# Performance work log

Measured on AMD Instinct MI355X. Metric: run time of the kernel, lower is better.

## Reference

```python
import jax, jax.numpy as jnp
import numpy as np

B, S, D, H, DFF = 4, 1024, 1024, 16, 4096
MAX_LEN = 1024
DK = D // H
EPS = 1e-5


def _ln(x, g, b):
    m = jnp.mean(x, axis=-1, keepdims=True)
    v = jnp.mean(jnp.square(x - m), axis=-1, keepdims=True)
    return (x - m) / jnp.sqrt(v + EPS) * g + b


def setup_inputs() -> dict:
    key = jax.random.key(0)
    ks = jax.random.split(key, 16)
    s = 0.02
    inp = {
        "x": jax.random.normal(ks[0], (B, S, D), jnp.float32),
        "wq": jax.random.normal(ks[1], (D, D), jnp.float32) * s,
        "bq": jnp.zeros((D,), jnp.float32),
        "wk": jax.random.normal(ks[2], (D, D), jnp.float32) * s,
        "bk": jnp.zeros((D,), jnp.float32),
        "wv": jax.random.normal(ks[3], (D, D), jnp.float32) * s,
        "bv": jnp.zeros((D,), jnp.float32),
        "wo": jax.random.normal(ks[4], (D, D), jnp.float32) * s,
        "bo": jnp.zeros((D,), jnp.float32),
        "rel_table": jax.random.normal(ks[5], (2 * MAX_LEN - 1, H), jnp.float32) * s,
        "ln1_g": jnp.ones((D,), jnp.float32),
        "ln1_b": jnp.zeros((D,), jnp.float32),
        "w1": jax.random.normal(ks[6], (D, DFF), jnp.float32) * s,
        "b1": jnp.zeros((DFF,), jnp.float32),
        "w2": jax.random.normal(ks[7], (DFF, D), jnp.float32) * s,
        "b2": jnp.zeros((D,), jnp.float32),
        "ln2_g": jnp.ones((D,), jnp.float32),
        "ln2_b": jnp.zeros((D,), jnp.float32),
        "mask": jnp.ones((B, 1, 1, S), jnp.int32),
    }
    return inp


def reference(x, wq, bq, wk, bk, wv, bv, wo, bo, rel_table,
              ln1_g, ln1_b, w1, b1, w2, b2, ln2_g, ln2_b, mask):
    # --- multi-head attention with relative position bias (post-LN encoder layer, eval mode) ---
    q = (x @ wq + bq).reshape(B, S, H, DK).transpose(0, 2, 1, 3)  # [B,H,S,dk]
    k = (x @ wk + bk).reshape(B, S, H, DK).transpose(0, 2, 1, 3)
    v = (x @ wv + bv).reshape(B, S, H, DK).transpose(0, 2, 1, 3)

    scores = jnp.einsum('bhqd,bhkd->bhqk', q, k) / jnp.sqrt(jnp.float32(DK))

    # relative position bias: table[(q - k + max_len - 1).clip] -> [1,H,S,S]
    coords = jnp.arange(S)[:, None] - jnp.arange(S)[None, :] + (MAX_LEN - 1)
    coords = jnp.clip(coords, 0, 2 * MAX_LEN - 2)
    bias = rel_table[coords]              # [S,S,H]
    scores = scores + bias.transpose(2, 0, 1)[None]

    scores = jnp.where(mask == 0, jnp.float32(-1e9), scores)
    attn = jax.nn.softmax(scores, axis=-1)
    ctx = jnp.einsum('bhqk,bhkd->bhqd', attn, v)
    ctx = ctx.transpose(0, 2, 1, 3).reshape(B, S, D)
    attn_out = ctx @ wo + bo

    x1 = _ln(x + attn_out, ln1_g, ln1_b)

    ff = jax.nn.relu(x1 @ w1 + b1) @ w2 + b2
    return _ln(x1 + ff, ln2_g, ln2_b)
```

## Files before the change

kernel.cpp:

```cpp
#include <hip/hip_runtime.h>
#include <hip/hip_bf16.h>

typedef __hip_bfloat16 bf16;
typedef __attribute__((ext_vector_type(8))) short short8;
typedef __attribute__((ext_vector_type(4))) float f32x4;

#define LOG2E 1.4426950408889634f

typedef const __attribute__((address_space(1))) void* gptr_t;
typedef __attribute__((address_space(3))) void* sptr_t;

__device__ __forceinline__ void async16(void* lds, const void* g) {
  __builtin_amdgcn_global_load_lds((gptr_t)g, (sptr_t)lds, 16, 0, 0);
}

__device__ __forceinline__ float bf2f(unsigned short u) {
  union { unsigned int i; float f; } c; c.i = ((unsigned int)u) << 16; return c.f;
}


__global__ __launch_bounds__(256) void prep_all(
    const float* __restrict__ x, const float* __restrict__ bq,
    const float* __restrict__ bk, const float* __restrict__ bv,
    const float* __restrict__ wq, const float* __restrict__ wk,
    const float* __restrict__ wv, const float* __restrict__ wo,
    const float* __restrict__ w1, const float* __restrict__ w2,
    bf16* __restrict__ xb, float* __restrict__ bqkv,
    bf16* __restrict__ dqkv, bf16* __restrict__ dwo,
    bf16* __restrict__ dw1, bf16* __restrict__ dw2) {
  const int bid = blockIdx.x;
  if (bid < 4096) {
    int i = (bid * 256 + threadIdx.x) * 4;
    float4 v = *(const float4*)(x + i);
    bf16 h4[4] = {__float2bfloat16(v.x), __float2bfloat16(v.y),
                  __float2bfloat16(v.z), __float2bfloat16(v.w)};
    *(uint2*)((unsigned short*)xb + i) = *(uint2*)h4;
    return;
  }
  if (bid == 16384) {
#pragma unroll
    for (int j = 0; j < 12; ++j) {
      int i = j * 256 + threadIdx.x;
      bqkv[i] = (i < 1024) ? bq[i] : (i < 2048 ? bk[i - 1024] : bv[i - 2048]);
    }
    return;
  }
  __shared__ float tl[32][33];
  const int tid = bid - 4096;
  const float* s;
  bf16* d;
  int NN, KK, n0, k0;
  if (tid < 4096) {
    int m = tid >> 10, tile = tid & 1023;
    s = m == 0 ? wq : m == 1 ? wk : m == 2 ? wv : wo;
    d = m < 3 ? dqkv + (size_t)m * 1024 * 1024 : dwo;
    NN = 1024; KK = 1024;
    n0 = (tile & 31) * 32; k0 = (tile >> 5) * 32;
  } else if (tid < 8192) {
    int tile = tid - 4096;
    s = w1; d = dw1; NN = 4096; KK = 1024;
    n0 = (tile & 127) * 32; k0 = (tile >> 7) * 32;
  } else {
    int tile = tid - 8192;
    s = w2; d = dw2; NN = 1024; KK = 4096;
    n0 = (tile & 31) * 32; k0 = (tile >> 5) * 32;
  }
  const int tx = threadIdx.x & 31, ty = threadIdx.x >> 5;
#pragma unroll
  for (int j = 0; j < 4; ++j)
    tl[ty + j * 8][tx] = s[(size_t)(k0 + ty + j * 8) * NN + n0 + tx];
  __syncthreads();
#pragma unroll
  for (int j = 0; j < 4; ++j)
    d[(size_t)(n0 + ty + j * 8) * KK + k0 + tx] =
        __float2bfloat16(tl[tx][ty + j * 8]);
}


template <int RELU, int VT>
__global__ __launch_bounds__(256) void gemm_bt(
    const bf16* __restrict__ A, const bf16* __restrict__ Bt,
    const float* __restrict__ bias, bf16* __restrict__ C,
    bf16* __restrict__ vt, int M, int N, int K) {
  __shared__ bf16 As[2][128 * 64];
  __shared__ bf16 Bs[2][128 * 64];
  const int t = threadIdx.x;
  const int w = t >> 6, l = t & 63;
  const int m0 = blockIdx.x * 128, n0 = blockIdx.y * 128;
  const int wr = (w >> 1) * 64, wc = (w & 1) * 64;
  const int srow = l >> 3, scol = l & 7;
  const int lm = l & 15, lq = l >> 4;

  f32x4 acc[4][4];
#pragma unroll
  for (int i = 0; i < 4; ++i)
#pragma unroll
    for (int j = 0; j < 4; ++j) acc[i][j] = (f32x4){0.f, 0.f, 0.f, 0.f};

  auto stage = [&](int k0, int d) {
#pragma unroll
    for (int p = 0; p < 4; ++p) {
      int row = p * 32 + w * 8 + srow;
      int gc = scol ^ (row & 7);
      async16(&As[d][(p * 32 + w * 8) * 64], A + (size_t)(m0 + row) * K + k0 + gc * 8);
      async16(&Bs[d][(p * 32 + w * 8) * 64], Bt + (size_t)(n0 + row) * K + k0 + gc * 8);
    }
  };

  stage(0, 0);
  const int niter = K >> 6;
  for (int it = 0; it < niter; ++it) {
    const int d = it & 1;
    __syncthreads();
    short8 af[2][4], bfr[2][4];
#pragma unroll
    for (int kk = 0; kk < 2; ++kk)
#pragma unroll
      for (int mi = 0; mi < 4; ++mi) {
        int rowa = wr + mi * 16 + lm;
        af[kk][mi] = *(const short8*)&As[d][rowa * 64 + (((kk * 4 + lq) ^ (rowa & 7)) << 3)];
        int rowb = wc + mi * 16 + lm;
        bfr[kk][mi] = *(const short8*)&Bs[d][rowb * 64 + (((kk * 4 + lq) ^ (rowb & 7)) << 3)];
      }
    if (it + 1 < niter) stage((it + 1) << 6, d ^ 1);
#pragma unroll
    for (int kk = 0; kk < 2; ++kk)
#pragma unroll
      for (int mi = 0; mi < 4; ++mi)
#pragma unroll
        for (int ni = 0; ni < 4; ++ni)
          acc[mi][ni] = __builtin_amdgcn_mfma_f32_16x16x32_bf16(
              af[kk][mi], bfr[kk][ni], acc[mi][ni], 0, 0, 0);
  }

#pragma unroll
  for (int mi = 0; mi < 4; ++mi)
#pragma unroll
    for (int ni = 0; ni < 4; ++ni) {
      int col = n0 + wc + ni * 16 + lm;
      int row0 = m0 + wr + mi * 16 + lq * 4;
      float bv = bias[col];
      float v[4];
#pragma unroll
      for (int r = 0; r < 4; ++r) {
        v[r] = acc[mi][ni][r] + bv;
        if (RELU) v[r] = fmaxf(v[r], 0.f);
        C[(size_t)(row0 + r) * N + col] = __float2bfloat16(v[r]);
      }
      if (VT && col >= 2048) {
        int vcol = col - 2048;
        int bh = (row0 >> 10) * 16 + (vcol >> 6);
        int dk = vcol & 63;
        int s = row0 & 1023;
        bf16 h4[4] = {__float2bfloat16(v[0]), __float2bfloat16(v[1]),
                      __float2bfloat16(v[2]), __float2bfloat16(v[3])};
        *(uint2*)&vt[((size_t)bh * 64 + dk) * 1024 + s] = *(uint2*)h4;
      }
    }
}

__global__ __launch_bounds__(256) void gemm_bt_splitk(
    const bf16* __restrict__ A, const bf16* __restrict__ Bt,
    bf16* __restrict__ P, int M, int N, int lda, int KS) {
  __shared__ bf16 As[2][128 * 64];
  __shared__ bf16 Bs[2][128 * 64];
  const int t = threadIdx.x;
  const int w = t >> 6, l = t & 63;
  const int m0 = blockIdx.x * 128, n0 = blockIdx.y * 128;
  const int kstart = blockIdx.z * KS;
  const int wr = (w >> 1) * 64, wc = (w & 1) * 64;
  const int srow = l >> 3, scol = l & 7;
  const int lm = l & 15, lq = l >> 4;

  f32x4 acc[4][4];
#pragma unroll
  for (int i = 0; i < 4; ++i)
#pragma unroll
    for (int j = 0; j < 4; ++j) acc[i][j] = (f32x4){0.f, 0.f, 0.f, 0.f};

  auto stage = [&](int k0, int d) {
#pragma unroll
    for (int p = 0; p < 4; ++p) {
      int row = p * 32 + w * 8 + srow;
      int gc = scol ^ (row & 7);
      async16(&As[d][(p * 32 + w * 8) * 64], A + (size_t)(m0 + row) * lda + k0 + gc * 8);
      async16(&Bs[d][(p * 32 + w * 8) * 64], Bt + (size_t)(n0 + row) * lda + k0 + gc * 8);
    }
  };

  stage(kstart, 0);
  const int niter = KS >> 6;
  for (int it = 0; it < niter; ++it) {
    const int d = it & 1;
    __syncthreads();
    short8 af[2][4], bfr[2][4];
#pragma unroll
    for (int kk = 0; kk < 2; ++kk)
#pragma unroll
      for (int mi = 0; mi < 4; ++mi) {
        int rowa = wr + mi * 16 + lm;
        af[kk][mi] = *(const short8*)&As[d][rowa * 64 + (((kk * 4 + lq) ^ (rowa & 7)) << 3)];
        int rowb = wc + mi * 16 + lm;
        bfr[kk][mi] = *(const short8*)&Bs[d][rowb * 64 + (((kk * 4 + lq) ^ (rowb & 7)) << 3)];
      }
    if (it + 1 < niter) stage(kstart + ((it + 1) << 6), d ^ 1);
#pragma unroll
    for (int kk = 0; kk < 2; ++kk)
#pragma unroll
      for (int mi = 0; mi < 4; ++mi)
#pragma unroll
        for (int ni = 0; ni < 4; ++ni)
          acc[mi][ni] = __builtin_amdgcn_mfma_f32_16x16x32_bf16(
              af[kk][mi], bfr[kk][ni], acc[mi][ni], 0, 0, 0);
  }
  bf16* Pz = P + (size_t)blockIdx.z * M * N;
#pragma unroll
  for (int mi = 0; mi < 4; ++mi)
#pragma unroll
    for (int r = 0; r < 4; ++r) {
      int row = m0 + wr + mi * 16 + lq * 4 + r;
#pragma unroll
      for (int ni = 0; ni < 4; ++ni) {
        int col = n0 + wc + ni * 16 + lm;
        Pz[(size_t)row * N + col] = __float2bfloat16(acc[mi][ni][r]);
      }
    }
}


__global__ __launch_bounds__(512, 4) void flash_attn(
    const bf16* __restrict__ qkv, const bf16* __restrict__ vt,
    const float* __restrict__ rel, const int* __restrict__ mask,
    bf16* __restrict__ ctx_part, float* __restrict__ lpart) {
  __shared__ bf16 Kl[2][64 * 64];
  __shared__ bf16 Vl[2][64 * 64];
  __shared__ bf16 Pl[128 * 64];
  __shared__ float bias_s[2][192];
  __shared__ float mask_s[2][64];

  const int t = threadIdx.x;
  const int w = t >> 6, l = t & 63;
  const int lm = l & 15, lq = l >> 4;
  const int qt = blockIdx.x, bh = blockIdx.y, z = blockIdx.z;
  const int b = bh >> 4, h = bh & 15;
  const int q0 = qt * 128;
  const int kt0 = z * 8;
  const int srow = l >> 3;
  const int gc = (l & 7) ^ srow;
  const int qq = w * 16 + lm;

  auto stage = [&](int d, int k0n) {
    async16(&Kl[d][w * 8 * 64],
            qkv + (size_t)(b * 1024 + k0n + w * 8 + srow) * 3072 + 1024 + h * 64 + gc * 8);
    async16(&Vl[d][w * 8 * 64],
            vt + ((size_t)bh * 64 + w * 8 + srow) * 1024 + k0n + gc * 8);
    if (t < 191) bias_s[d][t] = rel[(q0 - k0n + 960 + t) * 16 + h] * LOG2E;
    if (t < 64) mask_s[d][t] = (mask[b * 1024 + k0n + t] == 0) ? -1.44e9f : 0.f;
  };

#pragma unroll
  for (int p = 0; p < 2; ++p)
    async16(&Pl[(p * 64 + w * 8) * 64],
            qkv + (size_t)(b * 1024 + q0 + p * 64 + w * 8 + srow) * 3072 + h * 64 + gc * 8);
  stage(0, kt0 * 64);
  __syncthreads();

  short8 qf[2];
#pragma unroll
  for (int kk = 0; kk < 2; ++kk)
    qf[kk] = *(const short8*)&Pl[qq * 64 + (((kk * 4 + lq) ^ (lm & 7)) << 3)];
  __syncthreads();

  float l_acc = 0.f;
  f32x4 acc_o[4];
#pragma unroll
  for (int j = 0; j < 4; ++j) acc_o[j] = (f32x4){0.f, 0.f, 0.f, 0.f};

  const float C0 = 0.125f * LOG2E;

  for (int kt = kt0; kt < kt0 + 8; ++kt) {
    const int d = kt & 1;
    if (kt + 1 < kt0 + 8) stage(d ^ 1, (kt + 1) * 64);

    f32x4 sa[4];
#pragma unroll
    for (int i = 0; i < 4; ++i) sa[i] = (f32x4){0.f, 0.f, 0.f, 0.f};
#pragma unroll
    for (int kk = 0; kk < 2; ++kk) {
      short8 ak[4];
#pragma unroll
      for (int mi = 0; mi < 4; ++mi) {
        int row = mi * 16 + lm;
        ak[mi] = *(const short8*)&Kl[d][row * 64 + (((kk * 4 + lq) ^ (lm & 7)) << 3)];
      }
#pragma unroll
      for (int mi = 0; mi < 4; ++mi)
        sa[mi] = __builtin_amdgcn_mfma_f32_16x16x32_bf16(ak[mi], qf[kk], sa[mi], 0, 0, 0);
    }

    float m4[4][4];
#pragma unroll
    for (int mi = 0; mi < 4; ++mi)
      *(float4*)m4[mi] = *(const float4*)&mask_s[d][mi * 16 + lq * 4];
#pragma unroll
    for (int mi = 0; mi < 4; ++mi)
#pragma unroll
      for (int r = 0; r < 4; ++r) {
        int kl = mi * 16 + lq * 4 + r;
        float p = __builtin_amdgcn_exp2f(
            fmaf(sa[mi][r], C0, bias_s[d][qq - kl + 63] + m4[mi][r]));
        sa[mi][r] = p;
        l_acc += p;
      }

#pragma unroll
    for (int mi = 0; mi < 4; ++mi) {
      bf16 h4[4];
#pragma unroll
      for (int r = 0; r < 4; ++r) h4[r] = __float2bfloat16(sa[mi][r]);
      int chunk = mi * 2 + (lq >> 1);
      *(uint2*)&Pl[qq * 64 + ((chunk ^ (lm & 7)) << 3) + ((lq & 1) << 2)] =
          *(uint2*)h4;
    }

#pragma unroll
    for (int kk2 = 0; kk2 < 2; ++kk2) {
      short8 pf = *(const short8*)&Pl[qq * 64 + (((kk2 * 4 + lq) ^ (lm & 7)) << 3)];
      short8 vf[4];
#pragma unroll
      for (int ni = 0; ni < 4; ++ni) {
        int rowv = ni * 16 + lm;
        vf[ni] = *(const short8*)&Vl[d][rowv * 64 + (((kk2 * 4 + lq) ^ (lm & 7)) << 3)];
      }
#pragma unroll
      for (int ni = 0; ni < 4; ++ni)
        acc_o[ni] = __builtin_amdgcn_mfma_f32_16x16x32_bf16(pf, vf[ni], acc_o[ni], 0, 0, 0);
    }
    __syncthreads();
  }

  l_acc += __shfl_xor(l_acc, 16);
  l_acc += __shfl_xor(l_acc, 32);
  if (lq == 0)
    lpart[(size_t)z * 65536 + (size_t)bh * 1024 + q0 + qq] = l_acc;
  bf16* cp = ctx_part + (size_t)z * 4194304;
#pragma unroll
  for (int r = 0; r < 4; ++r) {
    int qx = w * 16 + lq * 4 + r;
    size_t rowbase = (size_t)(b * 1024 + q0 + qx) * 1024 + h * 64;
#pragma unroll
    for (int ni = 0; ni < 4; ++ni)
      cp[rowbase + ni * 16 + lm] = __float2bfloat16(acc_o[ni][r]);
  }
}

__global__ __launch_bounds__(256) void combine_ctx(
    const bf16* __restrict__ part, const float* __restrict__ lpart,
    bf16* __restrict__ ctx) {
  const int row = blockIdx.x, t = threadIdx.x;
  const size_t base = (size_t)row * 1024 + t * 4;
  const int b = row >> 10, s = row & 1023;
  const int h = t >> 4;
  float lsum = lpart[(size_t)(b * 16 + h) * 1024 + s] +
               lpart[65536 + (size_t)(b * 16 + h) * 1024 + s];
  float inv = 1.f / lsum;
  ushort4 p0 = *(const ushort4*)((const unsigned short*)part + base);
  ushort4 p1 = *(const ushort4*)((const unsigned short*)part + 4194304 + base);
  bf16 h4[4] = {__float2bfloat16((bf2f(p0.x) + bf2f(p1.x)) * inv),
                __float2bfloat16((bf2f(p0.y) + bf2f(p1.y)) * inv),
                __float2bfloat16((bf2f(p0.z) + bf2f(p1.z)) * inv),
                __float2bfloat16((bf2f(p0.w) + bf2f(p1.w)) * inv)};
  *(uint2*)((unsigned short*)ctx + base) = *(uint2*)h4;
}


template <typename RT, int NS>
__global__ __launch_bounds__(256) void ln_resid(
    const RT* __restrict__ xin, const bf16* __restrict__ part,
    const float* __restrict__ bias,
    const float* __restrict__ gw, const float* __restrict__ bw,
    float* __restrict__ outf, bf16* __restrict__ outb) {
  const int row = blockIdx.x, t = threadIdx.x;
  const size_t base = (size_t)row * 1024 + t * 4;
  float v0, v1, v2, v3;
  if constexpr (sizeof(RT) == 4) {
    float4 xv = *(const float4*)(xin + base);
    v0 = xv.x; v1 = xv.y; v2 = xv.z; v3 = xv.w;
  } else {
    ushort4 xv = *(const ushort4*)((const unsigned short*)xin + base);
    v0 = bf2f(xv.x); v1 = bf2f(xv.y); v2 = bf2f(xv.z); v3 = bf2f(xv.w);
  }
  float4 bi = *(const float4*)(bias + t * 4);
  v0 += bi.x; v1 += bi.y; v2 += bi.z; v3 += bi.w;
#pragma unroll
  for (int s = 0; s < NS; ++s) {
    const bf16* p = part + (size_t)s * 4194304 + base;
    ushort4 pv = *(const ushort4*)p;
    v0 += bf2f(pv.x); v1 += bf2f(pv.y); v2 += bf2f(pv.z); v3 += bf2f(pv.w);
  }
  float s1 = v0 + v1 + v2 + v3;
  float s2 = v0 * v0 + v1 * v1 + v2 * v2 + v3 * v3;
#pragma unroll
  for (int o = 1; o < 64; o <<= 1) {
    s1 += __shfl_xor(s1, o);
    s2 += __shfl_xor(s2, o);
  }
  __shared__ float red[8];
  const int w = t >> 6, l = t & 63;
  if (l == 0) { red[w] = s1; red[4 + w] = s2; }
  __syncthreads();
  float S1 = red[0] + red[1] + red[2] + red[3];
  float S2 = red[4] + red[5] + red[6] + red[7];
  float mean = S1 * (1.f / 1024.f);
  float var = S2 * (1.f / 1024.f) - mean * mean;
  float rstd = rsqrtf(var + 1e-5f);
  float4 gv = *(const float4*)(gw + t * 4);
  float4 bv = *(const float4*)(bw + t * 4);
  float o0 = (v0 - mean) * rstd * gv.x + bv.x;
  float o1 = (v1 - mean) * rstd * gv.y + bv.y;
  float o2 = (v2 - mean) * rstd * gv.z + bv.z;
  float o3 = (v3 - mean) * rstd * gv.w + bv.w;
  if (outf) {
    float4 ov = {o0, o1, o2, o3};
    *(float4*)(outf + base) = ov;
  }
  if (outb) {
    bf16 h4[4] = {__float2bfloat16(o0), __float2bfloat16(o1),
                  __float2bfloat16(o2), __float2bfloat16(o3)};
    *(uint2*)((unsigned short*)outb + base) = *(uint2*)h4;
  }
}


extern "C" void kernel_launch(void* const* d_in, const int* in_sizes, int n_in,
                              void* d_out, int out_size, void* d_ws, size_t ws_size,
                              hipStream_t stream) {
  (void)in_sizes; (void)n_in; (void)out_size; (void)ws_size;
  const float* x   = (const float*)d_in[0];
  const float* wq  = (const float*)d_in[1];
  const float* bq  = (const float*)d_in[2];
  const float* wk  = (const float*)d_in[3];
  const float* bk  = (const float*)d_in[4];
  const float* wv  = (const float*)d_in[5];
  const float* bv  = (const float*)d_in[6];
  const float* wo  = (const float*)d_in[7];
  const float* bo  = (const float*)d_in[8];
  const float* rel = (const float*)d_in[9];
  const float* g1  = (const float*)d_in[10];
  const float* be1 = (const float*)d_in[11];
  const float* w1  = (const float*)d_in[12];
  const float* b1  = (const float*)d_in[13];
  const float* w2  = (const float*)d_in[14];
  const float* b2  = (const float*)d_in[15];
  const float* g2  = (const float*)d_in[16];
  const float* be2 = (const float*)d_in[17];
  const int* mask  = (const int*)d_in[18];
  float* out = (float*)d_out;

  char* ws = (char*)d_ws;
  bf16*  xb       = (bf16*)(ws + 0);
  bf16*  wqkv_t   = (bf16*)(ws + 8388608);
  bf16*  wo_t     = (bf16*)(ws + 14680064);
  bf16*  w1_t     = (bf16*)(ws + 16777216);
  bf16*  ctx_b    = (bf16*)(ws + 25165824);
  bf16*  x1b      = (bf16*)(ws + 33554432);
  float* lpart    = (float*)(ws + 33554432);
  bf16*  qkv_b    = (bf16*)(ws + 41943040);
  bf16*  vtb      = (bf16*)(ws + 67108864);
  bf16*  part_wo  = (bf16*)(ws + 41943040);
  bf16*  h1       = (bf16*)(ws + 41943040);
  bf16*  part_ff  = (bf16*)(ws + 0);
  bf16*  w2_t     = (bf16*)(ws + 75497472);
  bf16*  ctx_part = (bf16*)(ws + 83886080);
  float* bqkv     = (float*)(ws + 100663296);

  prep_all<<<16385, 256, 0, stream>>>(x, bq, bk, bv, wq, wk, wv, wo, w1, w2,
                                      xb, bqkv, wqkv_t, wo_t, w1_t, w2_t);

  gemm_bt<0, 1><<<dim3(32, 24), 256, 0, stream>>>(
      xb, wqkv_t, bqkv, qkv_b, vtb, 4096, 3072, 1024);
  flash_attn<<<dim3(8, 64, 2), 512, 0, stream>>>(
      qkv_b, vtb, rel, mask, ctx_part, lpart);
  combine_ctx<<<4096, 256, 0, stream>>>(ctx_part, lpart, ctx_b);
  gemm_bt_splitk<<<dim3(32, 8, 2), 256, 0, stream>>>(
      ctx_b, wo_t, part_wo, 4096, 1024, 1024, 512);
  ln_resid<float, 2><<<4096, 256, 0, stream>>>(x, part_wo, bo, g1, be1, nullptr, x1b);
  gemm_bt<1, 0><<<dim3(32, 32), 256, 0, stream>>>(
      x1b, w1_t, b1, h1, nullptr, 4096, 4096, 1024);
  gemm_bt_splitk<<<dim3(32, 8, 2), 256, 0, stream>>>(
      h1, w2_t, part_ff, 4096, 1024, 4096, 2048);
  ln_resid<bf16, 2><<<4096, 256, 0, stream>>>(x1b, part_ff, b2, g2, be2, out, nullptr);
}
```

Measured before the change: 316.2 us.

## Double query tile per flash-attention block to reuse K/V staging

Each flash-attention block now handles 256 query rows instead of 128, so every wave computes two 16-row query subtiles against each staged K/V tile. The grid is halved along the query dimension, which halves the global loads of K, V, bias and mask per query and gives each wave more MFMA work per LDS fragment read. In exchange each thread holds more accumulators and registers, LDS per block grows, and there are only 512 blocks, so occupancy and latency hiding may drop.

```diff
diff --git a/kernel.cpp b/kernel.cpp
--- a/kernel.cpp
+++ b/kernel.cpp
@@ -234,8 +234,8 @@
     bf16* __restrict__ ctx_part, float* __restrict__ lpart) {
   __shared__ bf16 Kl[2][64 * 64];
   __shared__ bf16 Vl[2][64 * 64];
-  __shared__ bf16 Pl[128 * 64];
-  __shared__ float bias_s[2][192];
+  __shared__ bf16 Pl[256 * 64];
+  __shared__ float bias_s[2][320];
   __shared__ float mask_s[2][64];
 
   const int t = threadIdx.x;
@@ -243,38 +243,43 @@
   const int lm = l & 15, lq = l >> 4;
   const int qt = blockIdx.x, bh = blockIdx.y, z = blockIdx.z;
   const int b = bh >> 4, h = bh & 15;
-  const int q0 = qt * 128;
+  const int q0 = qt * 256;
   const int kt0 = z * 8;
   const int srow = l >> 3;
   const int gc = (l & 7) ^ srow;
-  const int qq = w * 16 + lm;
 
   auto stage = [&](int d, int k0n) {
     async16(&Kl[d][w * 8 * 64],
             qkv + (size_t)(b * 1024 + k0n + w * 8 + srow) * 3072 + 1024 + h * 64 + gc * 8);
     async16(&Vl[d][w * 8 * 64],
             vt + ((size_t)bh * 64 + w * 8 + srow) * 1024 + k0n + gc * 8);
-    if (t < 191) bias_s[d][t] = rel[(q0 - k0n + 960 + t) * 16 + h] * LOG2E;
+    if (t < 319) bias_s[d][t] = rel[(q0 - k0n + 960 + t) * 16 + h] * LOG2E;
     if (t < 64) mask_s[d][t] = (mask[b * 1024 + k0n + t] == 0) ? -1.44e9f : 0.f;
   };
 
 #pragma unroll
-  for (int p = 0; p < 2; ++p)
+  for (int p = 0; p < 4; ++p)
     async16(&Pl[(p * 64 + w * 8) * 64],
             qkv + (size_t)(b * 1024 + q0 + p * 64 + w * 8 + srow) * 3072 + h * 64 + gc * 8);
   stage(0, kt0 * 64);
   __syncthreads();
 
-  short8 qf[2];
-#pragma unroll
-  for (int kk = 0; kk < 2; ++kk)
-    qf[kk] = *(const short8*)&Pl[qq * 64 + (((kk * 4 + lq) ^ (lm & 7)) << 3)];
+  short8 qf[2][2];
+#pragma unroll
+  for (int ni = 0; ni < 2; ++ni)
+#pragma unroll
+    for (int kk = 0; kk < 2; ++kk) {
+      int row = w * 32 + ni * 16 + lm;
+      qf[ni][kk] = *(const short8*)&Pl[row * 64 + (((kk * 4 + lq) ^ (lm & 7)) << 3)];
+    }
   __syncthreads();
 
-  float l_acc = 0.f;
-  f32x4 acc_o[4];
-#pragma unroll
-  for (int j = 0; j < 4; ++j) acc_o[j] = (f32x4){0.f, 0.f, 0.f, 0.f};
+  float l_acc[2] = {0.f, 0.f};
+  f32x4 acc_o[2][4];
+#pragma unroll
+  for (int i = 0; i < 2; ++i)
+#pragma unroll
+    for (int j = 0; j < 4; ++j) acc_o[i][j] = (f32x4){0.f, 0.f, 0.f, 0.f};
 
   const float C0 = 0.125f * LOG2E;
 
@@ -282,9 +287,11 @@
     const int d = kt & 1;
     if (kt + 1 < kt0 + 8) stage(d ^ 1, (kt + 1) * 64);
 
-    f32x4 sa[4];
-#pragma unroll
-    for (int i = 0; i < 4; ++i) sa[i] = (f32x4){0.f, 0.f, 0.f, 0.f};
+    f32x4 sa[4][2];
+#pragma unroll
+    for (int i = 0; i < 4; ++i)
+#pragma unroll
+      for (int j = 0; j < 2; ++j) sa[i][j] = (f32x4){0.f, 0.f, 0.f, 0.f};
 #pragma unroll
     for (int kk = 0; kk < 2; ++kk) {
       short8 ak[4];
@@ -295,7 +302,10 @@
       }
 #pragma unroll
       for (int mi = 0; mi < 4; ++mi)
-        sa[mi] = __builtin_amdgcn_mfma_f32_16x16x32_bf16(ak[mi], qf[kk], sa[mi], 0, 0, 0);
+#pragma unroll
+        for (int ni = 0; ni < 2; ++ni)
+          sa[mi][ni] = __builtin_amdgcn_mfma_f32_16x16x32_bf16(
+              ak[mi], qf[ni][kk], sa[mi][ni], 0, 0, 0);
     }
 
     float m4[4][4];
@@ -305,27 +315,39 @@
 #pragma unroll
     for (int mi = 0; mi < 4; ++mi)
 #pragma unroll
-      for (int r = 0; r < 4; ++r) {
-        int kl = mi * 16 + lq * 4 + r;
-        float p = __builtin_amdgcn_exp2f(
-            fmaf(sa[mi][r], C0, bias_s[d][qq - kl + 63] + m4[mi][r]));
-        sa[mi][r] = p;
-        l_acc += p;
-      }
-
-#pragma unroll
-    for (int mi = 0; mi < 4; ++mi) {
-      bf16 h4[4];
-#pragma unroll
-      for (int r = 0; r < 4; ++r) h4[r] = __float2bfloat16(sa[mi][r]);
-      int chunk = mi * 2 + (lq >> 1);
-      *(uint2*)&Pl[qq * 64 + ((chunk ^ (lm & 7)) << 3) + ((lq & 1) << 2)] =
-          *(uint2*)h4;
-    }
+      for (int ni = 0; ni < 2; ++ni) {
+        int qq = w * 32 + ni * 16 + lm;
+#pragma unroll
+        for (int r = 0; r < 4; ++r) {
+          int kl = mi * 16 + lq * 4 + r;
+          float p = __builtin_amdgcn_exp2f(
+              fmaf(sa[mi][ni][r], C0, bias_s[d][qq - kl + 63] + m4[mi][r]));
+          sa[mi][ni][r] = p;
+          l_acc[ni] += p;
+        }
+      }
+
+#pragma unroll
+    for (int mi = 0; mi < 4; ++mi)
+#pragma unroll
+      for (int ni = 0; ni < 2; ++ni) {
+        bf16 h4[4];
+#pragma unroll
+        for (int r = 0; r < 4; ++r) h4[r] = __float2bfloat16(sa[mi][ni][r]);
+        int q = w * 32 + ni * 16 + lm;
+        int chunk = mi * 2 + (lq >> 1);
+        *(uint2*)&Pl[q * 64 + ((chunk ^ (lm & 7)) << 3) + ((lq & 1) << 2)] =
+            *(uint2*)h4;
+      }
 
 #pragma unroll
     for (int kk2 = 0; kk2 < 2; ++kk2) {
-      short8 pf = *(const short8*)&Pl[qq * 64 + (((kk2 * 4 + lq) ^ (lm & 7)) << 3)];
+      short8 pf[2];
+#pragma unroll
+      for (int mi2 = 0; mi2 < 2; ++mi2) {
+        int q = w * 32 + mi2 * 16 + lm;
+        pf[mi2] = *(const short8*)&Pl[q * 64 + (((kk2 * 4 + lq) ^ (lm & 7)) << 3)];
+      }
       short8 vf[4];
 #pragma unroll
       for (int ni = 0; ni < 4; ++ni) {
@@ -333,25 +355,36 @@
         vf[ni] = *(const short8*)&Vl[d][rowv * 64 + (((kk2 * 4 + lq) ^ (lm & 7)) << 3)];
       }
 #pragma unroll
+      for (int mi2 = 0; mi2 < 2; ++mi2)
+#pragma unroll
+        for (int ni = 0; ni < 4; ++ni)
+          acc_o[mi2][ni] = __builtin_amdgcn_mfma_f32_16x16x32_bf16(
+              pf[mi2], vf[ni], acc_o[mi2][ni], 0, 0, 0);
+    }
+    __syncthreads();
+  }
+
+#pragma unroll
+  for (int ni = 0; ni < 2; ++ni) {
+    l_acc[ni] += __shfl_xor(l_acc[ni], 16);
+    l_acc[ni] += __shfl_xor(l_acc[ni], 32);
+  }
+  if (lq == 0) {
+    size_t lb = (size_t)z * 65536 + (size_t)bh * 1024 + q0 + w * 32;
+    lpart[lb + lm] = l_acc[0];
+    lpart[lb + 16 + lm] = l_acc[1];
+  }
+  bf16* cp = ctx_part + (size_t)z * 4194304;
+#pragma unroll
+  for (int mi2 = 0; mi2 < 2; ++mi2)
+#pragma unroll
+    for (int r = 0; r < 4; ++r) {
+      int qx = w * 32 + mi2 * 16 + lq * 4 + r;
+      size_t rowbase = (size_t)(b * 1024 + q0 + qx) * 1024 + h * 64;
+#pragma unroll
       for (int ni = 0; ni < 4; ++ni)
-        acc_o[ni] = __builtin_amdgcn_mfma_f32_16x16x32_bf16(pf, vf[ni], acc_o[ni], 0, 0, 0);
-    }
-    __syncthreads();
-  }
-
-  l_acc += __shfl_xor(l_acc, 16);
-  l_acc += __shfl_xor(l_acc, 32);
-  if (lq == 0)
-    lpart[(size_t)z * 65536 + (size_t)bh * 1024 + q0 + qq] = l_acc;
-  bf16* cp = ctx_part + (size_t)z * 4194304;
-#pragma unroll
-  for (int r = 0; r < 4; ++r) {
-    int qx = w * 16 + lq * 4 + r;
-    size_t rowbase = (size_t)(b * 1024 + q0 + qx) * 1024 + h * 64;
-#pragma unroll
-    for (int ni = 0; ni < 4; ++ni)
-      cp[rowbase + ni * 16 + lm] = __float2bfloat16(acc_o[ni][r]);
-  }
+        cp[rowbase + ni * 16 + lm] = __float2bfloat16(acc_o[mi2][ni][r]);
+    }
 }
 
 __global__ __launch_bounds__(256) void combine_ctx(
@@ -479,7 +512,7 @@
 
   gemm_bt<0, 1><<<dim3(32, 24), 256, 0, stream>>>(
       xb, wqkv_t, bqkv, qkv_b, vtb, 4096, 3072, 1024);
-  flash_attn<<<dim3(8, 64, 2), 512, 0, stream>>>(
+  flash_attn<<<dim3(4, 64, 2), 512, 0, stream>>>(
       qkv_b, vtb, rel, mask, ctx_part, lpart);
   combine_ctx<<<4096, 256, 0, stream>>>(ctx_part, lpart, ctx_b);
   gemm_bt_splitk<<<dim3(32, 8, 2), 256, 0, stream>>>(
```

Result: no change. 317.9 us (+0.5%).
